# Kernel optimization log

Measured on AMD Instinct MI355X. Metric: run time of the kernel, lower is better.

The kernel has to match this reference:

```python
import jax, jax.numpy as jnp
import numpy as np

N_NODES = 50000
N_EDGES = 800000
IN_C = 128
OUT_C = 128


def setup_inputs() -> dict:
    key = jax.random.key(0)
    k1, k2, k3 = jax.random.split(key, 3)
    x = jax.random.normal(k1, (N_NODES, IN_C), dtype=jnp.float32)
    edge_index = jax.random.randint(k2, (2, N_EDGES), 0, N_NODES, dtype=jnp.int64)
    weight = jax.random.normal(k3, (IN_C, OUT_C), dtype=jnp.float32) * 0.01
    bias = jnp.zeros((OUT_C,), dtype=jnp.float32)
    return {"x": x, "edge_index": edge_index, "weight": weight, "bias": bias}


def reference(x, edge_index, weight, bias):
    num_nodes = x.shape[0]
    # add self-loops
    loop = jnp.arange(num_nodes, dtype=edge_index.dtype)
    src = jnp.concatenate([edge_index[0], loop])  # [E + N]
    dst = jnp.concatenate([edge_index[1], loop])  # [E + N]
    # in-degree (incl. self-loops) via scatter-add
    deg = jax.ops.segment_sum(jnp.ones_like(dst, dtype=x.dtype), dst,
                              num_segments=num_nodes)
    # deg >= 1 due to self-loops, but guard inf like the original
    deg_inv_sqrt = jnp.where(deg > 0, jax.lax.rsqrt(deg), 0.0)
    norm = deg_inv_sqrt[src] * deg_inv_sqrt[dst]  # [E + N]
    x_transformed = x @ weight  # [N, out_c]
    messages = x_transformed[src] * norm[:, None]  # [E + N, out_c]
    out = jax.ops.segment_sum(messages, dst, num_segments=num_nodes)
    return out + bias
```

## Files before the change

kernel.cpp:

```cpp
#include <hip/hip_runtime.h>

#define C 128
#define CHUNK 3200
#define SLOT 64
#define K4CAP 5120

typedef short bf16x8 __attribute__((ext_vector_type(8)));
typedef float f32x4 __attribute__((ext_vector_type(4)));

__device__ inline unsigned short f2bf(float f) {
    unsigned u = __float_as_uint(f);
    u += 0x7fffu + ((u >> 16) & 1u);
    return (unsigned short)(u >> 16);
}

__device__ inline unsigned pk2bf(float lo, float hi) {
    return (unsigned)f2bf(lo) | ((unsigned)f2bf(hi) << 16);
}

__device__ inline int wt_slot(int nn, int k8) {
    return (nn * 16 + k8) ^ (nn & 7);
}

__global__ __launch_bounds__(256) void kstage(
        const int* __restrict__ ei, int e,
        int* __restrict__ cnt, unsigned* __restrict__ staging,
        int nblocks, int nbuck,
        const float* __restrict__ W, unsigned* __restrict__ Wt) {
    __shared__ int h[256];
    __shared__ int c[256];
    __shared__ int bs[256];
    __shared__ unsigned rec[CHUNK];
    int b = blockIdx.x;
    int t = threadIdx.x;
    if (b >= nblocks) {
        int i = (b - nblocks) * 256 + t;
        if (i < 8192) {
            int nn = i & 127;
            int k = (i >> 7) * 2;
            unsigned pk = pk2bf(W[k * 128 + nn], W[(k + 1) * 128 + nn]);
            Wt[wt_slot(nn, k >> 3) * 4 + ((k & 7) >> 1)] = pk;
        }
        return;
    }
    h[t] = 0;
    __syncthreads();
    int base = b * CHUNK;
    int lim = min(CHUNK, e - base);
    for (int i = t; i < lim; i += 256)
        atomicAdd(&h[ei[e + base + i] >> 8], 1);
    __syncthreads();
    int v = h[t];
    c[t] = v;
    __syncthreads();
    for (int off = 1; off < 256; off <<= 1) {
        int u = (t >= off) ? c[t - off] : 0;
        __syncthreads();
        c[t] += u;
        __syncthreads();
    }
    int cbase = c[t] - v;
    if (t < nbuck) cnt[t * nblocks + b] = v;
    bs[t] = cbase;
    c[t] = cbase;
    __syncthreads();
    for (int i = t; i < lim; i += 256) {
        int s = ei[base + i];
        int d = ei[e + base + i];
        int pos = atomicAdd(&c[d >> 8], 1);
        rec[pos] = (unsigned)s | ((unsigned)(d & 255) << 16);
    }
    __syncthreads();
    int grp = t >> 4, l16 = t & 15;
    for (int g2 = grp; g2 < nbuck; g2 += 16) {
        int len = min(h[g2], SLOT);
        int rb = bs[g2];
        unsigned* segp = staging + ((size_t)g2 * nblocks + b) * SLOT;
        for (int k2 = l16; k2 < len; k2 += 16)
            segp[k2] = rec[rb + k2];
    }
}

union KMSM {
    struct { unsigned rec[K4CAP]; int sc[256]; int cu[256]; } fin;
    bf16x8 wt[2048];
};

__global__ __launch_bounds__(256) void kmid(
        const unsigned* __restrict__ staging, const int* __restrict__ cnt,
        int nblocks, int nbuck,
        int2* __restrict__ row_se, float* __restrict__ dis,
        unsigned short* __restrict__ srcs,
        const float* __restrict__ x, const unsigned* __restrict__ Wt,
        unsigned short* __restrict__ xts, int n) {
    __shared__ KMSM sm;
    int b = blockIdx.x, t = threadIdx.x;
    if (b < nbuck) {
        int g = b;
        int segc = (t < nblocks) ? min(cnt[g * nblocks + t], SLOT) : 0;
        sm.fin.sc[t] = segc;
        __syncthreads();
        for (int off = 1; off < 256; off <<= 1) {
            int u = (t >= off) ? sm.fin.sc[t - off] : 0;
            __syncthreads();
            sm.fin.sc[t] += u;
            __syncthreads();
        }
        int segbase = sm.fin.sc[t] - segc;
        int total = min(sm.fin.sc[255], K4CAP);
        const unsigned* segp = staging + ((size_t)g * nblocks + t) * SLOT;
        for (int k = 0; k < segc; k += 4) {
            uint4 w = *(const uint4*)(segp + k);
            int bd = segbase + k;
            if (bd < K4CAP) sm.fin.rec[bd] = w.x;
            if (k + 1 < segc && bd + 1 < K4CAP) sm.fin.rec[bd + 1] = w.y;
            if (k + 2 < segc && bd + 2 < K4CAP) sm.fin.rec[bd + 2] = w.z;
            if (k + 3 < segc && bd + 3 < K4CAP) sm.fin.rec[bd + 3] = w.w;
        }
        __syncthreads();
        sm.fin.sc[t] = 0;
        __syncthreads();
        for (int li = t; li < total; li += 256)
            atomicAdd(&sm.fin.sc[sm.fin.rec[li] >> 16], 1);
        __syncthreads();
        int v = sm.fin.sc[t];
        __syncthreads();
        for (int off = 1; off < 256; off <<= 1) {
            int u = (t >= off) ? sm.fin.sc[t - off] : 0;
            __syncthreads();
            sm.fin.sc[t] += u;
            __syncthreads();
        }
        int excl = sm.fin.sc[t] - v;
        int idx = g * 256 + t;
        int s0 = g * K4CAP;
        if (idx < n) {
            row_se[idx] = make_int2(s0 + excl, s0 + excl + v);
            dis[idx] = rsqrtf((float)(v + 1));
        }
        sm.fin.cu[t] = s0 + excl;
        __syncthreads();
        for (int li = t; li < total; li += 256) {
            unsigned r = sm.fin.rec[li];
            int pos = atomicAdd(&sm.fin.cu[r >> 16], 1);
            srcs[pos] = (unsigned short)(r & 0xffffu);
        }
    } else {
        uint4* dst4 = (uint4*)sm.wt;
        const uint4* src4 = (const uint4*)Wt;
#pragma unroll
        for (int i = 0; i < 8; ++i)
            dst4[t + i * 256] = src4[t + i * 256];
        __syncthreads();

        const int gb = b - nbuck;
        const int lane = t & 63;
        const int wave = t >> 6;
        const int m = lane & 15;
        const int q = lane >> 4;
        const int r0 = gb * 64 + wave * 16;
        const int row = r0 + m;
        const int rowc = (row < n) ? row : (n - 1);

        f32x4 acc[8];
#pragma unroll
        for (int nt = 0; nt < 8; ++nt) acc[nt] = (f32x4){0.f, 0.f, 0.f, 0.f};

#pragma unroll
        for (int kb = 0; kb < 4; ++kb) {
            const int k0 = kb * 32 + q * 8;
            const float4* xp = (const float4*)(x + (size_t)rowc * 128 + k0);
            float4 xa = xp[0];
            float4 xb = xp[1];
            union { unsigned u[4]; bf16x8 v; } af;
            af.u[0] = pk2bf(xa.x, xa.y);
            af.u[1] = pk2bf(xa.z, xa.w);
            af.u[2] = pk2bf(xb.x, xb.y);
            af.u[3] = pk2bf(xb.z, xb.w);
#pragma unroll
            for (int nt = 0; nt < 8; ++nt) {
                bf16x8 bf = sm.wt[wt_slot(nt * 16 + m, kb * 4 + q)];
                acc[nt] = __builtin_amdgcn_mfma_f32_16x16x32_bf16(af.v, bf, acc[nt], 0, 0, 0);
            }
        }

#pragma unroll
        for (int nt = 0; nt < 8; ++nt) {
            int col = nt * 16 + m;
#pragma unroll
            for (int r = 0; r < 4; ++r) {
                int gr = r0 + q * 4 + r;
                if (gr < n)
                    xts[(size_t)gr * 128 + col] = f2bf(acc[nt][r]);
            }
        }
    }
}

__device__ inline void fma8(float* a, uint4 w, float d) {
    a[0] += __uint_as_float(w.x << 16) * d;
    a[1] += __uint_as_float(w.x & 0xffff0000u) * d;
    a[2] += __uint_as_float(w.y << 16) * d;
    a[3] += __uint_as_float(w.y & 0xffff0000u) * d;
    a[4] += __uint_as_float(w.z << 16) * d;
    a[5] += __uint_as_float(w.z & 0xffff0000u) * d;
    a[6] += __uint_as_float(w.w << 16) * d;
    a[7] += __uint_as_float(w.w & 0xffff0000u) * d;
}

__global__ __launch_bounds__(256) void gather5(
        const int2* __restrict__ row_se,
        const unsigned short* __restrict__ srcs,
        const unsigned short* __restrict__ xts,
        const float* __restrict__ dis,
        const float* __restrict__ bias, float* __restrict__ out, int n) {
    int lane = threadIdx.x & 63;
    int wave = threadIdx.x >> 6;
    int sub = lane >> 5;
    int l32 = lane & 31;
    int e2 = l32 >> 4, q = l32 & 15;
    int node = blockIdx.x * 8 + wave * 2 + sub;
    if (node >= n) return;
    const uint4* x4 = (const uint4*)xts;
    int2 se = row_se[node];
    int end = se.y;
    float dself = dis[node];
    float a0[8] = {0, 0, 0, 0, 0, 0, 0, 0};
    float a1[8] = {0, 0, 0, 0, 0, 0, 0, 0};
    if (e2 == 0) fma8(a0, x4[node * 16 + q], dself);
    int j = se.x + e2;
    for (; j + 6 < end; j += 8) {
        int s0 = srcs[j], s1 = srcs[j + 2], s2 = srcs[j + 4], s3 = srcs[j + 6];
        float d0 = dis[s0], d1 = dis[s1], d2 = dis[s2], d3 = dis[s3];
        uint4 m0 = x4[s0 * 16 + q];
        uint4 m1 = x4[s1 * 16 + q];
        uint4 m2 = x4[s2 * 16 + q];
        uint4 m3 = x4[s3 * 16 + q];
        fma8(a0, m0, d0);
        fma8(a1, m1, d1);
        fma8(a0, m2, d2);
        fma8(a1, m3, d3);
    }
    for (; j + 2 < end; j += 4) {
        int s0 = srcs[j], s1 = srcs[j + 2];
        float d0 = dis[s0], d1 = dis[s1];
        uint4 m0 = x4[s0 * 16 + q];
        uint4 m1 = x4[s1 * 16 + q];
        fma8(a0, m0, d0);
        fma8(a1, m1, d1);
    }
    if (j < end) {
        int s = srcs[j];
        fma8(a0, x4[s * 16 + q], dis[s]);
    }
#pragma unroll
    for (int i = 0; i < 8; ++i) a0[i] += a1[i];
#pragma unroll
    for (int i = 0; i < 8; ++i)
        a0[i] += __shfl_xor(a0[i], 16, 64);
    if (e2 == 0) {
        const float4 b = ((const float4*)bias)[q * 2];
        float4 o;
        o.x = a0[0] * dself + b.x;
        o.y = a0[1] * dself + b.y;
        o.z = a0[2] * dself + b.z;
        o.w = a0[3] * dself + b.w;
        ((float4*)(out + (size_t)node * 128))[q * 2] = o;
    } else {
        const float4 b = ((const float4*)bias)[q * 2 + 1];
        float4 o;
        o.x = a0[4] * dself + b.x;
        o.y = a0[5] * dself + b.y;
        o.z = a0[6] * dself + b.z;
        o.w = a0[7] * dself + b.w;
        ((float4*)(out + (size_t)node * 128))[q * 2 + 1] = o;
    }
}

extern "C" void kernel_launch(void* const* d_in, const int* in_sizes, int n_in,
                              void* d_out, int out_size, void* d_ws, size_t ws_size,
                              hipStream_t stream) {
    const float* x    = (const float*)d_in[0];
    const int*   ei   = (const int*)d_in[1];
    const float* W    = (const float*)d_in[2];
    const float* bias = (const float*)d_in[3];
    float* out = (float*)d_out;

    const int n = in_sizes[0] / C;
    const int e = in_sizes[1] / 2;
    const int nblocks = (e + CHUNK - 1) / CHUNK;
    const int nbuck = (n + 255) >> 8;
    const int G = (n + 63) / 64;

    uintptr_t pa = ((uintptr_t)d_ws + 255) & ~(uintptr_t)255;
    char* p = (char*)pa;
    auto alloc = [&](size_t bytes) {
        char* r = p;
        p += (bytes + 255) & ~(size_t)255;
        return (void*)r;
    };
    int*      cnt     = (int*)alloc((size_t)nbuck * nblocks * 4);
    unsigned* staging = (unsigned*)alloc((size_t)nbuck * nblocks * SLOT * 4);
    int2*     row_se  = (int2*)alloc((size_t)n * 8);
    float*    dis     = (float*)alloc(n * 4);
    unsigned short* srcs = (unsigned short*)alloc((size_t)nbuck * K4CAP * 2);
    unsigned short* xts  = (unsigned short*)alloc((size_t)n * C * 2);
    unsigned* Wt      = (unsigned*)alloc(8192 * 4);

    kstage<<<nblocks + 64, 256, 0, stream>>>(ei, e, cnt, staging, nblocks,
                                             nbuck, W, Wt);
    kmid<<<nbuck + G, 256, 0, stream>>>(staging, cnt, nblocks, nbuck, row_se,
                                        dis, srcs, x, Wt, xts, n);
    gather5<<<(n + 7) / 8, 256, 0, stream>>>(row_se, srcs, xts, dis, bias, out, n);
}
```

Baseline: 133.5 us.

## Split transformed features into 32-channel slabs and gather slab by slab

The GEMM stage now writes the bf16 transformed features as four column slabs of 32 channels each. The gather kernel processes one slab at a time, so each pass touches a smaller working set that may stay cache-resident. In exchange, each lane issues 4-byte loads instead of 16-byte loads, and the edge indices and degree factors are re-read four times.

```diff
diff --git a/kernel.cpp b/kernel.cpp
--- a/kernel.cpp
+++ b/kernel.cpp
@@ -187,28 +187,23 @@
 #pragma unroll
         for (int nt = 0; nt < 8; ++nt) {
             int col = nt * 16 + m;
+            int kb2 = col >> 5, cc = col & 31;
 #pragma unroll
             for (int r = 0; r < 4; ++r) {
                 int gr = r0 + q * 4 + r;
                 if (gr < n)
-                    xts[(size_t)gr * 128 + col] = f2bf(acc[nt][r]);
+                    xts[(size_t)kb2 * n * 32 + (size_t)gr * 32 + cc] = f2bf(acc[nt][r]);
             }
         }
     }
 }
 
-__device__ inline void fma8(float* a, uint4 w, float d) {
-    a[0] += __uint_as_float(w.x << 16) * d;
-    a[1] += __uint_as_float(w.x & 0xffff0000u) * d;
-    a[2] += __uint_as_float(w.y << 16) * d;
-    a[3] += __uint_as_float(w.y & 0xffff0000u) * d;
-    a[4] += __uint_as_float(w.z << 16) * d;
-    a[5] += __uint_as_float(w.z & 0xffff0000u) * d;
-    a[6] += __uint_as_float(w.w << 16) * d;
-    a[7] += __uint_as_float(w.w & 0xffff0000u) * d;
-}
-
-__global__ __launch_bounds__(256) void gather5(
+__device__ inline void fma2(float* a, unsigned w, float d) {
+    a[0] += __uint_as_float(w << 16) * d;
+    a[1] += __uint_as_float(w & 0xffff0000u) * d;
+}
+
+__global__ __launch_bounds__(256) void gather6(
         const int2* __restrict__ row_se,
         const unsigned short* __restrict__ srcs,
         const unsigned short* __restrict__ xts,
@@ -218,62 +213,55 @@
     int wave = threadIdx.x >> 6;
     int sub = lane >> 5;
     int l32 = lane & 31;
-    int e2 = l32 >> 4, q = l32 & 15;
+    int grp = l32 >> 4, l16 = l32 & 15;
     int node = blockIdx.x * 8 + wave * 2 + sub;
     if (node >= n) return;
-    const uint4* x4 = (const uint4*)xts;
+    const unsigned* xu = (const unsigned*)xts;
     int2 se = row_se[node];
     int end = se.y;
     float dself = dis[node];
-    float a0[8] = {0, 0, 0, 0, 0, 0, 0, 0};
-    float a1[8] = {0, 0, 0, 0, 0, 0, 0, 0};
-    if (e2 == 0) fma8(a0, x4[node * 16 + q], dself);
-    int j = se.x + e2;
-    for (; j + 6 < end; j += 8) {
-        int s0 = srcs[j], s1 = srcs[j + 2], s2 = srcs[j + 4], s3 = srcs[j + 6];
-        float d0 = dis[s0], d1 = dis[s1], d2 = dis[s2], d3 = dis[s3];
-        uint4 m0 = x4[s0 * 16 + q];
-        uint4 m1 = x4[s1 * 16 + q];
-        uint4 m2 = x4[s2 * 16 + q];
-        uint4 m3 = x4[s3 * 16 + q];
-        fma8(a0, m0, d0);
-        fma8(a1, m1, d1);
-        fma8(a0, m2, d2);
-        fma8(a1, m3, d3);
-    }
-    for (; j + 2 < end; j += 4) {
-        int s0 = srcs[j], s1 = srcs[j + 2];
-        float d0 = dis[s0], d1 = dis[s1];
-        uint4 m0 = x4[s0 * 16 + q];
-        uint4 m1 = x4[s1 * 16 + q];
-        fma8(a0, m0, d0);
-        fma8(a1, m1, d1);
-    }
-    if (j < end) {
-        int s = srcs[j];
-        fma8(a0, x4[s * 16 + q], dis[s]);
-    }
-#pragma unroll
-    for (int i = 0; i < 8; ++i) a0[i] += a1[i];
-#pragma unroll
-    for (int i = 0; i < 8; ++i)
-        a0[i] += __shfl_xor(a0[i], 16, 64);
-    if (e2 == 0) {
-        const float4 b = ((const float4*)bias)[q * 2];
-        float4 o;
-        o.x = a0[0] * dself + b.x;
-        o.y = a0[1] * dself + b.y;
-        o.z = a0[2] * dself + b.z;
-        o.w = a0[3] * dself + b.w;
-        ((float4*)(out + (size_t)node * 128))[q * 2] = o;
-    } else {
-        const float4 b = ((const float4*)bias)[q * 2 + 1];
-        float4 o;
-        o.x = a0[4] * dself + b.x;
-        o.y = a0[5] * dself + b.y;
-        o.z = a0[6] * dself + b.z;
-        o.w = a0[7] * dself + b.w;
-        ((float4*)(out + (size_t)node * 128))[q * 2 + 1] = o;
+#pragma unroll
+    for (int kb = 0; kb < 4; ++kb) {
+        const unsigned* slab = xu + (size_t)kb * n * 16;
+        float a0[2] = {0, 0};
+        float a1[2] = {0, 0};
+        if (grp == 0) fma2(a0, slab[node * 16 + l16], dself);
+        int j = se.x + grp;
+        for (; j + 6 < end; j += 8) {
+            int s0 = srcs[j], s1 = srcs[j + 2], s2 = srcs[j + 4], s3 = srcs[j + 6];
+            float d0 = dis[s0], d1 = dis[s1], d2 = dis[s2], d3 = dis[s3];
+            unsigned w0 = slab[s0 * 16 + l16];
+            unsigned w1 = slab[s1 * 16 + l16];
+            unsigned w2 = slab[s2 * 16 + l16];
+            unsigned w3 = slab[s3 * 16 + l16];
+            fma2(a0, w0, d0);
+            fma2(a1, w1, d1);
+            fma2(a0, w2, d2);
+            fma2(a1, w3, d3);
+        }
+        for (; j + 2 < end; j += 4) {
+            int s0 = srcs[j], s1 = srcs[j + 2];
+            float d0 = dis[s0], d1 = dis[s1];
+            unsigned w0 = slab[s0 * 16 + l16];
+            unsigned w1 = slab[s1 * 16 + l16];
+            fma2(a0, w0, d0);
+            fma2(a1, w1, d1);
+        }
+        if (j < end) {
+            int s = srcs[j];
+            fma2(a0, slab[s * 16 + l16], dis[s]);
+        }
+        a0[0] += a1[0];
+        a0[1] += a1[1];
+        a0[0] += __shfl_xor(a0[0], 16, 64);
+        a0[1] += __shfl_xor(a0[1], 16, 64);
+        if (grp == 0) {
+            float2 bv = ((const float2*)bias)[kb * 16 + l16];
+            float2 o;
+            o.x = a0[0] * dself + bv.x;
+            o.y = a0[1] * dself + bv.y;
+            ((float2*)(out + (size_t)node * 128 + kb * 32))[l16] = o;
+        }
     }
 }
 
@@ -311,5 +299,5 @@
                                              nbuck, W, Wt);
     kmid<<<nbuck + G, 256, 0, stream>>>(staging, cnt, nblocks, nbuck, row_se,
                                         dis, srcs, x, Wt, xts, n);
-    gather5<<<(n + 7) / 8, 256, 0, stream>>>(row_se, srcs, xts, dis, bias, out, n);
-}
+    gather6<<<(n + 7) / 8, 256, 0, stream>>>(row_se, srcs, xts, dis, bias, out, n);
+}
```

Measured after the change: 165.1 us. 23.7% more time.
